# Kernel optimization log

Hardware: AMD Instinct MI355X
Metric: run time of the kernel (lower is better)

The kernel has to match this reference:

```python
import jax, jax.numpy as jnp
import numpy as np

B, T, D = 4, 2048, 1024
H = 4                      # fla GatedLinearAttention default num_heads
K = D; V = D               # expand_k = expand_v = 1
DK = K // H; DV = V // H   # 256 each
LOW = 16                   # gate_low_rank_dim default
GLN = 16.0                 # gate_logit_normalizer default


def _layernorm(x, w, b, eps=1e-5):
    mu = x.mean(-1, keepdims=True)
    xc = x - mu
    var = (xc * xc).mean(-1, keepdims=True)
    return xc * jax.lax.rsqrt(var + eps) * w + b


def _rmsnorm(x, w, eps=1e-5):
    ms = (x * x).mean(-1, keepdims=True)
    return x * jax.lax.rsqrt(ms + eps) * w


def _gla_scan(q, k, v, gk):
    # q,k,gk: [B,T,H,DK]; v: [B,T,H,DV]
    scale = DK ** -0.5
    qT = jnp.moveaxis(q * scale, 1, 0)  # [T,B,H,DK]
    kT = jnp.moveaxis(k, 1, 0)
    vT = jnp.moveaxis(v, 1, 0)
    gT = jnp.moveaxis(gk, 1, 0)

    def step(h, inp):
        qt, kt, vt, gt = inp  # [B,H,DK]/[B,H,DV]
        h = h * jnp.exp(gt)[..., None] + kt[..., :, None] * vt[..., None, :]
        o = jnp.einsum('bhk,bhkv->bhv', qt, h)
        return h, o

    h0 = jnp.zeros((q.shape[0], H, DK, DV), q.dtype)
    _, oT = jax.lax.scan(step, h0, (qT, kT, vT, gT))
    return jnp.moveaxis(oT, 0, 1)  # [B,T,H,DV]


def setup_inputs() -> dict:
    key = jax.random.key(0)
    ks = jax.random.split(key, 12)
    rn = lambda k, s: jax.random.normal(k, s, jnp.float32) * 0.02
    return {
        'x': jax.random.normal(ks[0], (B, T, D), jnp.float32),
        'ln1_w': jnp.ones((D,), jnp.float32), 'ln1_b': jnp.zeros((D,), jnp.float32),
        'Wq': rn(ks[1], (D, K)), 'Wk': rn(ks[2], (D, K)), 'Wv': rn(ks[3], (D, V)),
        'Wg': rn(ks[4], (D, V)),
        'Wgk1': rn(ks[5], (D, LOW)), 'Wgk2': rn(ks[6], (LOW, K)), 'bgk2': jnp.zeros((K,), jnp.float32),
        'rms_w': jnp.ones((DV,), jnp.float32),
        'Wo': rn(ks[7], (V, D)),
        'ln2_w': jnp.ones((D,), jnp.float32), 'ln2_b': jnp.zeros((D,), jnp.float32),
        'W1': rn(ks[8], (D, 3 * D)), 'b1': jnp.zeros((3 * D,), jnp.float32),
        'W2': rn(ks[9], (3 * D, D)), 'b2': jnp.zeros((D,), jnp.float32),
    }


def reference(x, ln1_w, ln1_b, Wq, Wk, Wv, Wg, Wgk1, Wgk2, bgk2, rms_w, Wo,
              ln2_w, ln2_b, W1, b1, W2, b2):
    b, t = x.shape[0], x.shape[1]
    xn = _layernorm(x, ln1_w, ln1_b)
    q = (xn @ Wq).reshape(b, t, H, DK)
    k = (xn @ Wk).reshape(b, t, H, DK)
    v = (xn @ Wv).reshape(b, t, H, DV)
    # low-rank forget gate: logsigmoid / gate_logit_normalizer
    gk = (jax.nn.log_sigmoid((xn @ Wgk1) @ Wgk2 + bgk2) / GLN).reshape(b, t, H, DK)
    o = _gla_scan(q, k, v, gk)                      # [B,T,H,DV]
    g = (xn @ Wg).reshape(b, t, H, DV)              # output gate
    o = _rmsnorm(o, rms_w) * (g * jax.nn.sigmoid(g))  # gated RMSNorm (swish gate)
    o = o.reshape(b, t, V) @ Wo
    x = x + o
    xn2 = _layernorm(x, ln2_w, ln2_b)
    h = jax.nn.leaky_relu(xn2 @ W1 + b1, 0.01)
    h = h * h                                        # LeakyReLU^2
    x = x + (h @ W2 + b2)
    return x
```

## Files before the change

kernel.cpp:

```cpp
#include <hip/hip_runtime.h>
#include <math.h>

#define BB 4
#define TT 2048
#define DD 1024
#define HH 4
#define DK 256
#define DV 256
#define RR 8192
#define CHK 64
#define NCHK 32
#define SS ((size_t)RR * DD)

typedef __bf16 bf16x8 __attribute__((ext_vector_type(8)));
typedef float f32x4 __attribute__((ext_vector_type(4)));

static __device__ inline unsigned short f2bf(float f) {
  unsigned int u = __float_as_uint(f);
  unsigned int r = (u + 0x7fffu + ((u >> 16) & 1u)) >> 16;
  return (unsigned short)r;
}
static __device__ inline float bf2f(unsigned short h) {
  return __uint_as_float(((unsigned int)h) << 16);
}

static __device__ __forceinline__ void gload16(const unsigned short* g,
                                               unsigned short* l) {
  __builtin_amdgcn_global_load_lds(
      (const __attribute__((address_space(1))) void*)g,
      (__attribute__((address_space(3))) void*)l, 16, 0, 0);
}

__global__ __launch_bounds__(256) void ln_kernel(const float* __restrict__ x,
                                                 const float* __restrict__ w,
                                                 const float* __restrict__ b,
                                                 unsigned short* __restrict__ yb) {
  int row = blockIdx.x;
  const float* xr = x + (size_t)row * DD;
  unsigned short* ybr = yb + (size_t)row * DD;
  int tid = threadIdx.x;

  float4 v = ((const float4*)xr)[tid];
  float s = v.x + v.y + v.z + v.w;
  float ss = v.x * v.x + v.y * v.y + v.z * v.z + v.w * v.w;
#pragma unroll
  for (int o = 32; o > 0; o >>= 1) {
    s += __shfl_down(s, o);
    ss += __shfl_down(ss, o);
  }
  __shared__ float ls[4], lss[4];
  int wid = tid >> 6;
  if ((tid & 63) == 0) { ls[wid] = s; lss[wid] = ss; }
  __syncthreads();
  float sum = ls[0] + ls[1] + ls[2] + ls[3];
  float sumsq = lss[0] + lss[1] + lss[2] + lss[3];
  float mu = sum * (1.0f / DD);
  float var = sumsq * (1.0f / DD) - mu * mu;
  float rs = rsqrtf(var + 1e-5f);

  float4 wv = ((const float4*)w)[tid];
  float4 bv = ((const float4*)b)[tid];
  ushort4 ob;
  ob.x = f2bf((v.x - mu) * rs * wv.x + bv.x);
  ob.y = f2bf((v.y - mu) * rs * wv.y + bv.y);
  ob.z = f2bf((v.z - mu) * rs * wv.z + bv.z);
  ob.w = f2bf((v.w - mu) * rs * wv.w + bv.w);
  ((ushort4*)ybr)[tid] = ob;
}

__global__ __launch_bounds__(256) void transpose_cast(const float* __restrict__ W,
                                                      unsigned short* __restrict__ Wt,
                                                      int K, int N) {
  __shared__ float t[32][33];
  int k0 = blockIdx.y * 32, n0 = blockIdx.x * 32;
  int tid = threadIdx.x;
  int tx = tid & 31, ty = tid >> 5;
#pragma unroll
  for (int i = 0; i < 4; ++i)
    t[ty + i * 8][tx] = W[(size_t)(k0 + ty + i * 8) * N + n0 + tx];
  __syncthreads();
#pragma unroll
  for (int i = 0; i < 4; ++i)
    Wt[(size_t)(n0 + ty + i * 8) * K + k0 + tx] = f2bf(t[tx][ty + i * 8]);
}

struct P5 {
  const float* w[5];
  unsigned short* o[5];
};
__global__ __launch_bounds__(256) void transpose5(P5 p) {
  __shared__ float t[32][33];
  int z = blockIdx.z;
  const float* W = p.w[z];
  unsigned short* Wt = p.o[z];
  int k0 = blockIdx.y * 32, n0 = blockIdx.x * 32;
  int tid = threadIdx.x;
  int tx = tid & 31, ty = tid >> 5;
#pragma unroll
  for (int i = 0; i < 4; ++i)
    t[ty + i * 8][tx] = W[(size_t)(k0 + ty + i * 8) * 1024 + n0 + tx];
  __syncthreads();
#pragma unroll
  for (int i = 0; i < 4; ++i)
    Wt[(size_t)(n0 + ty + i * 8) * 1024 + k0 + tx] = f2bf(t[tx][ty + i * 8]);
}

template <int EPI, int OUTBF>
__global__ __launch_bounds__(256) void gemm_bf16(
    const unsigned short* __restrict__ A,
    const unsigned short* __restrict__ Bt,
    const float* __restrict__ bias, const float* __restrict__ Res,
    void* __restrict__ Cv, int M, int N, int K) {
  __shared__ unsigned short As[2][128 * 64];
  __shared__ unsigned short Bs[2][128 * 64];
  int tid = threadIdx.x;
  int nwg = gridDim.x * gridDim.y;
  int wg = blockIdx.y * gridDim.x + blockIdx.x;
  int cpx = nwg >> 3;
  wg = (wg & 7) * cpx + (wg >> 3);
  int m0 = (wg / gridDim.x) * 128, n0 = (wg % gridDim.x) * 128;
  int lane = tid & 63;
  int w64 = tid & 192;
  int wid = tid >> 6;
  int wm = (wid >> 1) * 64, wn = (wid & 1) * 64;
  int fr = lane & 15, fq = lane >> 4;

  f32x4 acc[4][4] = {};

  auto STAGE = [&](int buf, int k0) {
#pragma unroll
    for (int j = 0; j < 4; ++j) {
      int gl = j * 256 + tid;
      int row = gl >> 3;
      int gs = (gl & 7) ^ (row & 7);
      gload16(&A[(size_t)(m0 + row) * K + k0 + gs * 8],
              &As[buf][(size_t)(j * 256 + w64) * 8]);
      gload16(&Bt[(size_t)(n0 + row) * K + k0 + gs * 8],
              &Bs[buf][(size_t)(j * 256 + w64) * 8]);
    }
  };

  STAGE(0, 0);
  asm volatile("s_waitcnt vmcnt(0)");
  __syncthreads();

  int cur = 0;
  for (int k0 = 0; k0 < K; k0 += 64) {
    if (k0 + 64 < K) STAGE(cur ^ 1, k0 + 64);

#pragma unroll
    for (int ph = 0; ph < 2; ++ph) {
      bf16x8 af[4], bv[4];
#pragma unroll
      for (int i = 0; i < 4; ++i) {
        int ra = wm + i * 16 + fr;
        af[i] = *(const bf16x8*)&As[cur][ra * 64 + (((ph * 4 + fq) ^ (ra & 7)) * 8)];
        int rb = wn + i * 16 + fr;
        bv[i] = *(const bf16x8*)&Bs[cur][rb * 64 + (((ph * 4 + fq) ^ (rb & 7)) * 8)];
      }
#pragma unroll
      for (int i = 0; i < 4; ++i)
#pragma unroll
        for (int jj = 0; jj < 4; ++jj)
          acc[i][jj] = __builtin_amdgcn_mfma_f32_16x16x32_bf16(af[i], bv[jj],
                                                               acc[i][jj], 0, 0, 0);
    }
    __syncthreads();
    cur ^= 1;
  }

  int col = lane & 15;
  int rbase = (lane >> 4) * 4;
#pragma unroll
  for (int i = 0; i < 4; ++i) {
#pragma unroll
    for (int j = 0; j < 4; ++j) {
      int n = n0 + wn + j * 16 + col;
      float bvv = (EPI == 2 || EPI == 4) ? bias[n] : 0.0f;
#pragma unroll
      for (int r = 0; r < 4; ++r) {
        int m = m0 + wm + i * 16 + rbase + r;
        float vv = acc[i][j][r] + bvv;
        if (EPI == 2) {
          float t = vv > 0.0f ? vv : 0.01f * vv;
          vv = t * t;
        }
        if (EPI == 3 || EPI == 4) vv += Res[(size_t)m * N + n];
        if (EPI == 5) {
          ((unsigned short*)Cv)[(size_t)(n >> 10) * SS + (size_t)m * 1024 +
                                (n & 1023)] = f2bf(vv);
        } else if (OUTBF) {
          ((unsigned short*)Cv)[(size_t)m * N + n] = f2bf(vv);
        } else {
          ((float*)Cv)[(size_t)m * N + n] = vv;
        }
      }
    }
  }
}

__global__ __launch_bounds__(256) void gk_kernel(const unsigned short* __restrict__ xn,
                                                 const float* __restrict__ Wgk1,
                                                 const float* __restrict__ Wgk2,
                                                 const float* __restrict__ bgk2,
                                                 unsigned short* __restrict__ gk) {
  __shared__ unsigned short Xs[16 * 1024];
  __shared__ unsigned short W1s[1024 * 16];
  __shared__ float Ts[16][16];
  int r0 = blockIdx.x * 16;
  int tid = threadIdx.x;

#pragma unroll
  for (int i = 0; i < 16; ++i) {
    int idx = tid + i * 256;
    ((ushort4*)Xs)[idx] = ((const ushort4*)(xn + (size_t)r0 * 1024))[idx];
  }
#pragma unroll
  for (int i = 0; i < 16; ++i) {
    int idx = tid + i * 256;
    float4 w = ((const float4*)Wgk1)[idx];
    ushort4 hh;
    hh.x = f2bf(w.x); hh.y = f2bf(w.y); hh.z = f2bf(w.z); hh.w = f2bf(w.w);
    ((ushort4*)W1s)[idx] = hh;
  }
  __syncthreads();

  {
    int r = tid >> 4, part = tid & 15;
    float t16[16];
#pragma unroll
    for (int j = 0; j < 16; ++j) t16[j] = 0.0f;
    for (int dd = 0; dd < 64; ++dd) {
      int d = dd * 16 + part;
      float xv = bf2f(Xs[r * 1024 + d]);
      const ushort4* wr = (const ushort4*)&W1s[d * 16];
#pragma unroll
      for (int q4 = 0; q4 < 4; ++q4) {
        ushort4 w = wr[q4];
        t16[q4 * 4 + 0] += xv * bf2f(w.x);
        t16[q4 * 4 + 1] += xv * bf2f(w.y);
        t16[q4 * 4 + 2] += xv * bf2f(w.z);
        t16[q4 * 4 + 3] += xv * bf2f(w.w);
      }
    }
#pragma unroll
    for (int j = 0; j < 16; ++j) {
      float s = t16[j];
      s += __shfl_xor(s, 1);
      s += __shfl_xor(s, 2);
      s += __shfl_xor(s, 4);
      s += __shfl_xor(s, 8);
      t16[j] = s;
    }
    if (part == 0) {
#pragma unroll
      for (int j = 0; j < 16; ++j) Ts[r][j] = t16[j];
    }
  }
  __syncthreads();

  {
    float w2[16][4];
#pragma unroll
    for (int j = 0; j < 16; ++j) {
      float4 wv = *(const float4*)&Wgk2[(size_t)j * 1024 + tid * 4];
      w2[j][0] = wv.x; w2[j][1] = wv.y; w2[j][2] = wv.z; w2[j][3] = wv.w;
    }
    float4 bv = *(const float4*)&bgk2[tid * 4];
    float bb[4] = {bv.x, bv.y, bv.z, bv.w};
#pragma unroll
    for (int r = 0; r < 16; ++r) {
      ushort4 outv;
      unsigned short* op = (unsigned short*)&outv;
#pragma unroll
      for (int jj = 0; jj < 4; ++jj) {
        float z = bb[jj];
#pragma unroll
        for (int j = 0; j < 16; ++j) z += Ts[r][j] * w2[j][jj];
        float lsg = fminf(z, 0.0f) - log1pf(expf(-fabsf(z)));
        op[jj] = f2bf(lsg * (1.0f / 16.0f));
      }
      *(ushort4*)&Xs[r * 1024 + tid * 4] = outv;
    }
  }
  __syncthreads();
#pragma unroll
  for (int i = 0; i < 16; ++i) {
    int idx = tid + i * 256;
    ((ushort4*)(gk + (size_t)r0 * 1024))[idx] = ((const ushort4*)Xs)[idx];
  }
}

__global__ __launch_bounds__(256) void gate_chunk(const unsigned short* __restrict__ gk,
                                                  unsigned short* __restrict__ q,
                                                  unsigned short* __restrict__ k,
                                                  float* __restrict__ ebC) {
  int bid = blockIdx.x;
  int c = bid & 31;
  int h = (bid >> 5) & 3;
  int b = bid >> 7;
  int tid = threadIdx.x;
  size_t base = ((size_t)b * TT + c * CHK) * 1024 + h * 256 + tid;

  float cums[64];
#pragma unroll
  for (int t = 0; t < 64; ++t) cums[t] = bf2f(gk[base + (size_t)t * 1024]);
  float cum = 0.0f;
#pragma unroll
  for (int t = 0; t < 64; ++t) {
    cum += cums[t];
    cums[t] = cum;
  }
  ebC[((b * 4 + h) * NCHK + c) * 256 + tid] = expf(cum);

  const float scale = 0.0625f;
#pragma unroll
  for (int t = 0; t < 64; ++t) {
    size_t a = base + (size_t)t * 1024;
    q[a] = f2bf(bf2f(q[a]) * expf(cums[t]) * scale);
    k[a] = f2bf(bf2f(k[a]) * expf(-cums[t]));
  }
}

template <int WITHE>
__global__ __launch_bounds__(256) void trans_kernel(const unsigned short* __restrict__ in,
                                                    const float* __restrict__ ebC,
                                                    unsigned short* __restrict__ outT) {
  __shared__ unsigned short T[64][68];
  int bid = blockIdx.x;
  int dkt = bid & 3;
  int ct = (bid >> 2) & 31;
  int bh = bid >> 7;
  int b = bh >> 2, h = bh & 3;
  int tid = threadIdx.x;
  int r = tid >> 4;
  int c4 = (tid & 15) * 4;
  size_t srcbase = ((size_t)b * TT + ct * 64) * 1024 + h * 256 + dkt * 64;
#pragma unroll
  for (int i = 0; i < 4; ++i)
    *(ushort4*)&T[r + i * 16][c4] =
        *(const ushort4*)&in[srcbase + (size_t)(r + i * 16) * 1024 + c4];
  __syncthreads();
  size_t outbase = (size_t)bh * 524288 + (size_t)(dkt * 64) * 2048 + ct * 64;
  const float* ep = ebC + ((size_t)bh * 32 + ct) * 256 + dkt * 64;
#pragma unroll
  for (int i = 0; i < 4; ++i) {
    int dkl = r + i * 16;
    float e = WITHE ? ep[dkl] : 1.0f;
    ushort4 o;
    o.x = f2bf(bf2f(T[c4 + 0][dkl]) * e);
    o.y = f2bf(bf2f(T[c4 + 1][dkl]) * e);
    o.z = f2bf(bf2f(T[c4 + 2][dkl]) * e);
    o.w = f2bf(bf2f(T[c4 + 3][dkl]) * e);
    *(ushort4*)&outT[outbase + (size_t)dkl * 2048 + c4] = o;
  }
}

__global__ __launch_bounds__(256) void u_gemm(const unsigned short* __restrict__ khatT,
                                              const unsigned short* __restrict__ vT,
                                              unsigned short* __restrict__ UT) {
  __shared__ unsigned short As[128 * 64];
  __shared__ unsigned short Bs[128 * 64];
  int tid = threadIdx.x;
  int bid = blockIdx.x;
  int tile = bid & 3;
  int bhc = bid >> 2;
  int bh = bhc >> 5, c = bhc & 31;
  int m0 = (tile >> 1) * 128, n0 = (tile & 1) * 128;
  const unsigned short* Ab = vT + (size_t)bh * 524288 + c * 64;
  const unsigned short* Bb = khatT + (size_t)bh * 524288 + c * 64;
  unsigned short* Cb = UT + (size_t)bhc * 65536;

  int lane = tid & 63;
  int w64 = tid & 192;
  int wid = tid >> 6;
  int wm = (wid >> 1) * 64, wn = (wid & 1) * 64;
  int fr = lane & 15, fq = lane >> 4;

  f32x4 acc[4][4] = {};

#pragma unroll
  for (int j = 0; j < 4; ++j) {
    int gl = j * 256 + tid;
    int row = gl >> 3;
    int gs = (gl & 7) ^ (row & 7);
    gload16(&Ab[(size_t)(m0 + row) * 2048 + gs * 8],
            &As[(size_t)(j * 256 + w64) * 8]);
    gload16(&Bb[(size_t)(n0 + row) * 2048 + gs * 8],
            &Bs[(size_t)(j * 256 + w64) * 8]);
  }
  __syncthreads();

#pragma unroll
  for (int ph = 0; ph < 2; ++ph) {
    bf16x8 af[4], bv[4];
#pragma unroll
    for (int i = 0; i < 4; ++i) {
      int ra = wm + i * 16 + fr;
      af[i] = *(const bf16x8*)&As[ra * 64 + (((ph * 4 + fq) ^ (ra & 7)) * 8)];
      int rb = wn + i * 16 + fr;
      bv[i] = *(const bf16x8*)&Bs[rb * 64 + (((ph * 4 + fq) ^ (rb & 7)) * 8)];
    }
#pragma unroll
    for (int i = 0; i < 4; ++i)
#pragma unroll
      for (int jj = 0; jj < 4; ++jj)
        acc[i][jj] = __builtin_amdgcn_mfma_f32_16x16x32_bf16(af[i], bv[jj],
                                                             acc[i][jj], 0, 0, 0);
  }

  int col = lane & 15;
  int rbase = (lane >> 4) * 4;
#pragma unroll
  for (int i = 0; i < 4; ++i)
#pragma unroll
    for (int j = 0; j < 4; ++j) {
      int n = n0 + wn + j * 16 + col;
#pragma unroll
      for (int r = 0; r < 4; ++r) {
        int m = m0 + wm + i * 16 + rbase + r;
        Cb[(size_t)m * 256 + n] = f2bf(acc[i][j][r]);
      }
    }
}

__global__ __launch_bounds__(256) void hscan(unsigned short* __restrict__ UH,
                                             const float* __restrict__ ebC) {
  int bid = blockIdx.x;
  int bh = bid >> 8, dv = bid & 255;
  int tid = threadIdx.x;
  size_t base = ((size_t)bh * NCHK) * 65536 + (size_t)dv * 256 + tid;
  const float* ebb = ebC + (size_t)bh * NCHK * 256 + tid;

  float u[32], e[32];
#pragma unroll
  for (int c = 0; c < 32; ++c) u[c] = bf2f(UH[base + (size_t)c * 65536]);
#pragma unroll
  for (int c = 0; c < 32; ++c) e[c] = ebb[c * 256];
  float h = 0.0f;
#pragma unroll
  for (int c = 0; c < 32; ++c) {
    UH[base + (size_t)c * 65536] = f2bf(h);
    h = e[c] * h + u[c];
  }
}

__global__ __launch_bounds__(256) void attn_fused(
    const unsigned short* __restrict__ qt, const unsigned short* __restrict__ kt,
    const unsigned short* __restrict__ vT, const unsigned short* __restrict__ HT,
    const unsigned short* __restrict__ gp, const float* __restrict__ rw,
    unsigned short* __restrict__ og) {
  __shared__ unsigned short Qs[64 * 264];
  __shared__ unsigned short KVH[256 * 72];
  __shared__ unsigned short Sb[64 * 64];
  __shared__ float red[64][4];

  int bid = blockIdx.x;
  int c = bid & 31;
  int bh = bid >> 5;
  int b = bh >> 2, h = bh & 3;
  size_t rowbase = ((size_t)b * TT + c * 64) * 1024 + h * 256;
  size_t vtbase = (size_t)bh * 524288 + c * 64;
  size_t htbase = ((size_t)(bh * 32 + c)) * 65536;
  int tid = threadIdx.x;
  int lane = tid & 63;
  int w = tid >> 6;
  int fr = lane & 15, fq = lane >> 4;

#pragma unroll
  for (int i = 0; i < 8; ++i) {
    int gg = tid + i * 256;
    int row = gg >> 5, gc = gg & 31;
    *(bf16x8*)&Qs[row * 264 + gc * 8] =
        *(const bf16x8*)&qt[rowbase + (size_t)row * 1024 + gc * 8];
    *(bf16x8*)&KVH[row * 264 + gc * 8] =
        *(const bf16x8*)&kt[rowbase + (size_t)row * 1024 + gc * 8];
  }
  __syncthreads();

  {
    f32x4 accs[4] = {};
#pragma unroll
    for (int ks = 0; ks < 8; ++ks) {
      bf16x8 af = *(const bf16x8*)&Qs[(w * 16 + fr) * 264 + ks * 32 + fq * 8];
#pragma unroll
      for (int si = 0; si < 4; ++si) {
        bf16x8 bf_ = *(const bf16x8*)&KVH[(si * 16 + fr) * 264 + ks * 32 + fq * 8];
        accs[si] = __builtin_amdgcn_mfma_f32_16x16x32_bf16(af, bf_, accs[si], 0, 0, 0);
      }
    }
#pragma unroll
    for (int si = 0; si < 4; ++si) {
#pragma unroll
      for (int r = 0; r < 4; ++r) {
        int t = w * 16 + fq * 4 + r;
        int s = si * 16 + fr;
        float val = (s <= t) ? accs[si][r] : 0.0f;
        Sb[t * 64 + (((s >> 3) ^ (t & 7)) * 8) + (s & 7)] = f2bf(val);
      }
    }
  }
  __syncthreads();

#pragma unroll
  for (int i = 0; i < 8; ++i) {
    int gg = tid + i * 256;
    int dv = gg >> 3, gc = gg & 7;
    *(bf16x8*)&KVH[dv * 72 + gc * 8] =
        *(const bf16x8*)&vT[vtbase + (size_t)dv * 2048 + gc * 8];
  }
  __syncthreads();

  int dv0 = w * 64;
  f32x4 acc[4][4] = {};

#pragma unroll
  for (int ks = 0; ks < 2; ++ks) {
    bf16x8 af[4], bv[4];
#pragma unroll
    for (int ti = 0; ti < 4; ++ti) {
      int t = ti * 16 + fr;
      af[ti] = *(const bf16x8*)&Sb[t * 64 + (((ks * 4 + fq) ^ (t & 7)) * 8)];
    }
#pragma unroll
    for (int nj = 0; nj < 4; ++nj)
      bv[nj] = *(const bf16x8*)&KVH[(dv0 + nj * 16 + fr) * 72 + ks * 32 + fq * 8];
#pragma unroll
    for (int ti = 0; ti < 4; ++ti)
#pragma unroll
      for (int nj = 0; nj < 4; ++nj)
        acc[ti][nj] = __builtin_amdgcn_mfma_f32_16x16x32_bf16(af[ti], bv[nj],
                                                              acc[ti][nj], 0, 0, 0);
  }

  for (int k4 = 0; k4 < 4; ++k4) {
    __syncthreads();
#pragma unroll
    for (int i = 0; i < 8; ++i) {
      int gg = tid + i * 256;
      int dv = gg >> 3, gc = gg & 7;
      *(bf16x8*)&KVH[dv * 72 + gc * 8] =
          *(const bf16x8*)&HT[htbase + (size_t)dv * 256 + k4 * 64 + gc * 8];
    }
    __syncthreads();
#pragma unroll
    for (int ks = 0; ks < 2; ++ks) {
      bf16x8 af[4], bv[4];
#pragma unroll
      for (int ti = 0; ti < 4; ++ti)
        af[ti] = *(const bf16x8*)&Qs[(ti * 16 + fr) * 264 + k4 * 64 + ks * 32 + fq * 8];
#pragma unroll
      for (int nj = 0; nj < 4; ++nj)
        bv[nj] = *(const bf16x8*)&KVH[(dv0 + nj * 16 + fr) * 72 + ks * 32 + fq * 8];
#pragma unroll
      for (int ti = 0; ti < 4; ++ti)
#pragma unroll
        for (int nj = 0; nj < 4; ++nj)
          acc[ti][nj] = __builtin_amdgcn_mfma_f32_16x16x32_bf16(af[ti], bv[nj],
                                                                acc[ti][nj], 0, 0, 0);
    }
  }

  float rstd[4][4];
#pragma unroll
  for (int ti = 0; ti < 4; ++ti) {
#pragma unroll
    for (int r = 0; r < 4; ++r) {
      float s = 0.0f;
#pragma unroll
      for (int nj = 0; nj < 4; ++nj) {
        float v = acc[ti][nj][r];
        s += v * v;
      }
      s += __shfl_xor(s, 1);
      s += __shfl_xor(s, 2);
      s += __shfl_xor(s, 4);
      s += __shfl_xor(s, 8);
      rstd[ti][r] = s;
    }
  }
  if (fr == 0) {
#pragma unroll
    for (int ti = 0; ti < 4; ++ti)
#pragma unroll
      for (int r = 0; r < 4; ++r)
        red[ti * 16 + fq * 4 + r][w] = rstd[ti][r];
  }
  __syncthreads();
#pragma unroll
  for (int ti = 0; ti < 4; ++ti) {
#pragma unroll
    for (int r = 0; r < 4; ++r) {
      int t = ti * 16 + fq * 4 + r;
      float tot = red[t][0] + red[t][1] + red[t][2] + red[t][3];
      rstd[ti][r] = rsqrtf(tot * (1.0f / 256.0f) + 1e-5f);
    }
  }
#pragma unroll
  for (int ti = 0; ti < 4; ++ti) {
#pragma unroll
    for (int nj = 0; nj < 4; ++nj) {
      int dv = dv0 + nj * 16 + fr;
      float rwv = rw[dv];
#pragma unroll
      for (int r = 0; r < 4; ++r) {
        int t = ti * 16 + fq * 4 + r;
        float gv = bf2f(gp[rowbase + (size_t)t * 1024 + dv]);
        float sw = gv / (1.0f + expf(-gv));
        og[rowbase + (size_t)t * 1024 + dv] =
            f2bf(acc[ti][nj][r] * rstd[ti][r] * rwv * sw);
      }
    }
  }
}

extern "C" void kernel_launch(void* const* d_in, const int* in_sizes, int n_in,
                              void* d_out, int out_size, void* d_ws,
                              size_t ws_size, hipStream_t stream) {
  const float* x = (const float*)d_in[0];
  const float* ln1_w = (const float*)d_in[1];
  const float* ln1_b = (const float*)d_in[2];
  const float* Wq = (const float*)d_in[3];
  const float* Wk = (const float*)d_in[4];
  const float* Wv = (const float*)d_in[5];
  const float* Wg = (const float*)d_in[6];
  const float* Wgk1 = (const float*)d_in[7];
  const float* Wgk2 = (const float*)d_in[8];
  const float* bgk2 = (const float*)d_in[9];
  const float* rms_w = (const float*)d_in[10];
  const float* Wo = (const float*)d_in[11];
  const float* ln2_w = (const float*)d_in[12];
  const float* ln2_b = (const float*)d_in[13];
  const float* W1 = (const float*)d_in[14];
  const float* b1 = (const float*)d_in[15];
  const float* W2 = (const float*)d_in[16];
  const float* b2 = (const float*)d_in[17];
  float* out = (float*)d_out;

  const size_t S = SS;
  unsigned short* actb = (unsigned short*)d_ws;
  unsigned short* qb = actb + S;
  unsigned short* kb = qb + S;
  unsigned short* vb = kb + S;
  unsigned short* gb = vb + S;
  unsigned short* gkb = gb + S;
  unsigned short* ogb = gkb + S;
  unsigned short* UH = ogb + 2 * S;
  float* ebC = (float*)(UH + 4 * S);
  unsigned short* Wqkvgt = (unsigned short*)(ebC + 131072);
  unsigned short* Wot = Wqkvgt + 4194304;
  unsigned short* W1t = Wot + 1048576;
  unsigned short* W2t = W1t + 3145728;
  unsigned short* khatT = gkb;
  unsigned short* vT = actb;
  float* x1 = (float*)kb;
  unsigned short* hb = UH;

  dim3 blk(256);

  P5 p5;
  p5.w[0] = Wq;  p5.o[0] = Wqkvgt;
  p5.w[1] = Wk;  p5.o[1] = Wqkvgt + 1048576;
  p5.w[2] = Wv;  p5.o[2] = Wqkvgt + 2097152;
  p5.w[3] = Wg;  p5.o[3] = Wqkvgt + 3145728;
  p5.w[4] = Wo;  p5.o[4] = Wot;
  transpose5<<<dim3(32, 32, 5), blk, 0, stream>>>(p5);
  transpose_cast<<<dim3(96, 32), blk, 0, stream>>>(W1, W1t, 1024, 3072);
  transpose_cast<<<dim3(32, 96), blk, 0, stream>>>(W2, W2t, 3072, 1024);

  ln_kernel<<<RR, blk, 0, stream>>>(x, ln1_w, ln1_b, actb);

  dim3 g4096(4096 / 128, RR / 128);
  gemm_bf16<5, 1><<<g4096, blk, 0, stream>>>(actb, Wqkvgt, nullptr, nullptr, qb,
                                             RR, 4096, 1024);

  gk_kernel<<<RR / 16, blk, 0, stream>>>(actb, Wgk1, Wgk2, bgk2, gkb);

  gate_chunk<<<BB * HH * NCHK, blk, 0, stream>>>(gkb, qb, kb, ebC);

  trans_kernel<1><<<16 * 32 * 4, blk, 0, stream>>>(kb, ebC, khatT);
  trans_kernel<0><<<16 * 32 * 4, blk, 0, stream>>>(vb, ebC, vT);

  u_gemm<<<16 * NCHK * 4, blk, 0, stream>>>(khatT, vT, UH);
  hscan<<<16 * 256, blk, 0, stream>>>(UH, ebC);

  attn_fused<<<16 * NCHK, blk, 0, stream>>>(qb, kb, vT, UH, gb, rms_w, ogb);

  dim3 g1024(1024 / 128, RR / 128);
  gemm_bf16<3, 0><<<g1024, blk, 0, stream>>>(ogb, Wot, nullptr, x, x1, RR, 1024, 1024);

  ln_kernel<<<RR, blk, 0, stream>>>(x1, ln2_w, ln2_b, actb);

  dim3 g3072(3072 / 128, RR / 128);
  gemm_bf16<2, 1><<<g3072, blk, 0, stream>>>(actb, W1t, b1, nullptr, hb, RR, 3072, 1024);

  gemm_bf16<4, 0><<<g1024, blk, 0, stream>>>(hb, W2t, b2, x1, out, RR, 1024, 3072);
}
```

Measured before the change: 426.1 us.

## Replace 128x128 GEMM with 256x256-tile, 512-thread software-pipelined MFMA kernel

Replaces the bf16 GEMM used for the QKVG, output, and both MLP projections with a 256x256 output tile computed by 8 waves. Loads are split into half-tile stages interleaved with the MFMA phases, with explicit barriers, waitcnt, sched_barrier and setprio to overlap global-to-LDS copies with compute. The aim is more data reuse per loaded tile and better latency hiding. In exchange it uses 128KB of LDS, holds 128 accumulator registers per lane, launches fewer workgroups (only 128 for the N=1024 GEMMs), and depends on fragile hand-written synchronisation.

```diff
diff --git a/kernel.cpp b/kernel.cpp
--- a/kernel.cpp
+++ b/kernel.cpp
@@ -106,73 +106,118 @@
 }
 
 template <int EPI, int OUTBF>
-__global__ __launch_bounds__(256) void gemm_bf16(
+__global__ __launch_bounds__(512, 2) void gemm256(
     const unsigned short* __restrict__ A,
     const unsigned short* __restrict__ Bt,
     const float* __restrict__ bias, const float* __restrict__ Res,
     void* __restrict__ Cv, int M, int N, int K) {
-  __shared__ unsigned short As[2][128 * 64];
-  __shared__ unsigned short Bs[2][128 * 64];
+  __shared__ unsigned short As[2][2][128 * 64];
+  __shared__ unsigned short Bs[2][2][128 * 64];
   int tid = threadIdx.x;
   int nwg = gridDim.x * gridDim.y;
   int wg = blockIdx.y * gridDim.x + blockIdx.x;
   int cpx = nwg >> 3;
   wg = (wg & 7) * cpx + (wg >> 3);
-  int m0 = (wg / gridDim.x) * 128, n0 = (wg % gridDim.x) * 128;
+  int m0 = (wg / gridDim.x) * 256, n0 = (wg % gridDim.x) * 256;
   int lane = tid & 63;
-  int w64 = tid & 192;
+  int w64 = tid & 448;
   int wid = tid >> 6;
-  int wm = (wid >> 1) * 64, wn = (wid & 1) * 64;
+  int wm = (wid >> 2) * 128;
+  int wn = (wid & 3) * 64;
   int fr = lane & 15, fq = lane >> 4;
 
-  f32x4 acc[4][4] = {};
-
-  auto STAGE = [&](int buf, int k0) {
-#pragma unroll
-    for (int j = 0; j < 4; ++j) {
-      int gl = j * 256 + tid;
+  f32x4 acc[8][4] = {};
+  int nt = K >> 6;
+
+  auto STAGEH = [&](int mat, int h, int t) {
+    if (t >= nt) return;
+    int d = t & 1;
+    const unsigned short* G = mat ? Bt : A;
+    int base0 = (mat ? n0 : m0) + h * 128;
+    unsigned short* L = mat ? &Bs[d][h][0] : &As[d][h][0];
+    int k0 = t * 64;
+#pragma unroll
+    for (int j = 0; j < 2; ++j) {
+      int gl = j * 512 + tid;
       int row = gl >> 3;
       int gs = (gl & 7) ^ (row & 7);
-      gload16(&A[(size_t)(m0 + row) * K + k0 + gs * 8],
-              &As[buf][(size_t)(j * 256 + w64) * 8]);
-      gload16(&Bt[(size_t)(n0 + row) * K + k0 + gs * 8],
-              &Bs[buf][(size_t)(j * 256 + w64) * 8]);
+      gload16(&G[(size_t)(base0 + row) * K + k0 + gs * 8],
+              &L[(size_t)(j * 512 + w64) * 8]);
     }
   };
 
-  STAGE(0, 0);
-  asm volatile("s_waitcnt vmcnt(0)");
-  __syncthreads();
-
-  int cur = 0;
-  for (int k0 = 0; k0 < K; k0 += 64) {
-    if (k0 + 64 < K) STAGE(cur ^ 1, k0 + 64);
-
-#pragma unroll
-    for (int ph = 0; ph < 2; ++ph) {
-      bf16x8 af[4], bv[4];
-#pragma unroll
-      for (int i = 0; i < 4; ++i) {
-        int ra = wm + i * 16 + fr;
-        af[i] = *(const bf16x8*)&As[cur][ra * 64 + (((ph * 4 + fq) ^ (ra & 7)) * 8)];
-        int rb = wn + i * 16 + fr;
-        bv[i] = *(const bf16x8*)&Bs[cur][rb * 64 + (((ph * 4 + fq) ^ (rb & 7)) * 8)];
-      }
-#pragma unroll
-      for (int i = 0; i < 4; ++i)
-#pragma unroll
-        for (int jj = 0; jj < 4; ++jj)
-          acc[i][jj] = __builtin_amdgcn_mfma_f32_16x16x32_bf16(af[i], bv[jj],
-                                                               acc[i][jj], 0, 0, 0);
-    }
-    __syncthreads();
-    cur ^= 1;
+  STAGEH(0, 0, 0); STAGEH(0, 1, 0);
+  STAGEH(1, 0, 0); STAGEH(1, 1, 0);
+  STAGEH(1, 0, 1); STAGEH(1, 1, 1);
+  asm volatile("s_waitcnt vmcnt(0)" ::: "memory");
+  __builtin_amdgcn_sched_barrier(0);
+  __builtin_amdgcn_s_barrier();
+  __builtin_amdgcn_sched_barrier(0);
+
+  for (int u = 0; u < nt; u += 2) {
+#pragma unroll
+    for (int hh = 0; hh < 2; ++hh) {
+      int d = hh;
+      bf16x8 breg[4][2];
+#pragma unroll
+      for (int p = 0; p < 4; ++p) {
+        bf16x8 af[2][2];
+        if (p == 0) {
+#pragma unroll
+          for (int j = 0; j < 4; ++j) {
+            int rb = wn + j * 16 + fr;
+            int hB = rb >> 7, rr = rb & 127;
+#pragma unroll
+            for (int ks = 0; ks < 2; ++ks)
+              breg[j][ks] = *(const bf16x8*)&Bs[d][hB][rr * 64 +
+                                (((ks * 4 + fq) ^ (rr & 7)) * 8)];
+          }
+        }
+#pragma unroll
+        for (int i = 0; i < 2; ++i) {
+          int ra = wm + (2 * p + i) * 16 + fr;
+          int hA = ra >> 7, rr = ra & 127;
+#pragma unroll
+          for (int ks = 0; ks < 2; ++ks)
+            af[i][ks] = *(const bf16x8*)&As[d][hA][rr * 64 +
+                              (((ks * 4 + fq) ^ (rr & 7)) * 8)];
+        }
+        if (hh == 0) {
+          if (p == 0) STAGEH(0, 0, u + 1);
+          if (p == 1) { STAGEH(0, 1, u + 1); STAGEH(1, 0, u + 2); }
+          if (p == 2) STAGEH(1, 1, u + 2);
+        } else {
+          if (p == 0) STAGEH(0, 0, u + 2);
+          if (p == 1) STAGEH(0, 1, u + 2);
+          if (p == 2) STAGEH(1, 0, u + 3);
+          if (p == 3) STAGEH(1, 1, u + 3);
+        }
+        __builtin_amdgcn_sched_barrier(0);
+        __builtin_amdgcn_s_barrier();
+        asm volatile("s_waitcnt lgkmcnt(0)" ::: "memory");
+        __builtin_amdgcn_sched_barrier(0);
+        __builtin_amdgcn_s_setprio(1);
+#pragma unroll
+        for (int i = 0; i < 2; ++i)
+#pragma unroll
+          for (int j = 0; j < 4; ++j)
+#pragma unroll
+            for (int ks = 0; ks < 2; ++ks)
+              acc[2 * p + i][j] = __builtin_amdgcn_mfma_f32_16x16x32_bf16(
+                  af[i][ks], breg[j][ks], acc[2 * p + i][j], 0, 0, 0);
+        __builtin_amdgcn_s_setprio(0);
+        if (p == 3) asm volatile("s_waitcnt vmcnt(4)" ::: "memory");
+        __builtin_amdgcn_sched_barrier(0);
+        __builtin_amdgcn_s_barrier();
+        __builtin_amdgcn_sched_barrier(0);
+      }
+    }
   }
 
   int col = lane & 15;
   int rbase = (lane >> 4) * 4;
 #pragma unroll
-  for (int i = 0; i < 4; ++i) {
+  for (int i = 0; i < 8; ++i) {
 #pragma unroll
     for (int j = 0; j < 4; ++j) {
       int n = n0 + wn + j * 16 + col;
@@ -182,8 +227,8 @@
         int m = m0 + wm + i * 16 + rbase + r;
         float vv = acc[i][j][r] + bvv;
         if (EPI == 2) {
-          float t = vv > 0.0f ? vv : 0.01f * vv;
-          vv = t * t;
+          float t2 = vv > 0.0f ? vv : 0.01f * vv;
+          vv = t2 * t2;
         }
         if (EPI == 3 || EPI == 4) vv += Res[(size_t)m * N + n];
         if (EPI == 5) {
@@ -657,6 +702,7 @@
   unsigned short* hb = UH;
 
   dim3 blk(256);
+  dim3 blk512(512);
 
   P5 p5;
   p5.w[0] = Wq;  p5.o[0] = Wqkvgt;
@@ -670,9 +716,9 @@
 
   ln_kernel<<<RR, blk, 0, stream>>>(x, ln1_w, ln1_b, actb);
 
-  dim3 g4096(4096 / 128, RR / 128);
-  gemm_bf16<5, 1><<<g4096, blk, 0, stream>>>(actb, Wqkvgt, nullptr, nullptr, qb,
-                                             RR, 4096, 1024);
+  dim3 g4096(4096 / 256, RR / 256);
+  gemm256<5, 1><<<g4096, blk512, 0, stream>>>(actb, Wqkvgt, nullptr, nullptr, qb,
+                                              RR, 4096, 1024);
 
   gk_kernel<<<RR / 16, blk, 0, stream>>>(actb, Wgk1, Wgk2, bgk2, gkb);
 
@@ -686,13 +732,13 @@
 
   attn_fused<<<16 * NCHK, blk, 0, stream>>>(qb, kb, vT, UH, gb, rms_w, ogb);
 
-  dim3 g1024(1024 / 128, RR / 128);
-  gemm_bf16<3, 0><<<g1024, blk, 0, stream>>>(ogb, Wot, nullptr, x, x1, RR, 1024, 1024);
+  dim3 g1024(1024 / 256, RR / 256);
+  gemm256<3, 0><<<g1024, blk512, 0, stream>>>(ogb, Wot, nullptr, x, x1, RR, 1024, 1024);
 
   ln_kernel<<<RR, blk, 0, stream>>>(x1, ln2_w, ln2_b, actb);
 
-  dim3 g3072(3072 / 128, RR / 128);
-  gemm_bf16<2, 1><<<g3072, blk, 0, stream>>>(actb, W1t, b1, nullptr, hb, RR, 3072, 1024);
-
-  gemm_bf16<4, 0><<<g1024, blk, 0, stream>>>(hb, W2t, b2, x1, out, RR, 1024, 3072);
-}
+  dim3 g3072(3072 / 256, RR / 256);
+  gemm256<2, 1><<<g3072, blk512, 0, stream>>>(actb, W1t, b1, nullptr, hb, RR, 3072, 1024);
+
+  gemm256<4, 0><<<g1024, blk512, 0, stream>>>(hb, W2t, b2, x1, out, RR, 1024, 3072);
+}
```

New measurement: 453.8 us. +6.5%, slower.

## Fuse chunk state GEMM and scan into one kernel; shrink GEMM K-tile

Applied to the files above, without the earlier changes.

The separate per-chunk U GEMM and the hidden-state scan are replaced by one kernel. Each block owns a 64x64 (dv, dk) tile of the state and walks the 32 chunks in order. It computes the chunk update with MFMA, keeps the running state in fp32 registers and writes each chunk's prefix state. This removes the round trip of writing the U buffer to global memory and reading it back, and drops a launch. The cost is only 256 blocks with a serial chunk loop, which exposes per-chunk latency. Separately, the main bf16 GEMM K-step drops from 64 to 32, halving shared memory per block to allow more resident blocks, at the cost of twice as many barriers and loop iterations.

```diff
diff --git a/kernel.cpp b/kernel.cpp
--- a/kernel.cpp
+++ b/kernel.cpp
@@ -111,8 +111,8 @@
     const unsigned short* __restrict__ Bt,
     const float* __restrict__ bias, const float* __restrict__ Res,
     void* __restrict__ Cv, int M, int N, int K) {
-  __shared__ unsigned short As[2][128 * 64];
-  __shared__ unsigned short Bs[2][128 * 64];
+  __shared__ unsigned short As[2][128 * 32];
+  __shared__ unsigned short Bs[2][128 * 32];
   int tid = threadIdx.x;
   int nwg = gridDim.x * gridDim.y;
   int wg = blockIdx.y * gridDim.x + blockIdx.x;
@@ -129,10 +129,10 @@
 
   auto STAGE = [&](int buf, int k0) {
 #pragma unroll
-    for (int j = 0; j < 4; ++j) {
+    for (int j = 0; j < 2; ++j) {
       int gl = j * 256 + tid;
-      int row = gl >> 3;
-      int gs = (gl & 7) ^ (row & 7);
+      int row = gl >> 2;
+      int gs = (gl & 3) ^ (row & 3);
       gload16(&A[(size_t)(m0 + row) * K + k0 + gs * 8],
               &As[buf][(size_t)(j * 256 + w64) * 8]);
       gload16(&Bt[(size_t)(n0 + row) * K + k0 + gs * 8],
@@ -145,26 +145,23 @@
   __syncthreads();
 
   int cur = 0;
-  for (int k0 = 0; k0 < K; k0 += 64) {
-    if (k0 + 64 < K) STAGE(cur ^ 1, k0 + 64);
-
-#pragma unroll
-    for (int ph = 0; ph < 2; ++ph) {
-      bf16x8 af[4], bv[4];
-#pragma unroll
-      for (int i = 0; i < 4; ++i) {
-        int ra = wm + i * 16 + fr;
-        af[i] = *(const bf16x8*)&As[cur][ra * 64 + (((ph * 4 + fq) ^ (ra & 7)) * 8)];
-        int rb = wn + i * 16 + fr;
-        bv[i] = *(const bf16x8*)&Bs[cur][rb * 64 + (((ph * 4 + fq) ^ (rb & 7)) * 8)];
-      }
-#pragma unroll
-      for (int i = 0; i < 4; ++i)
-#pragma unroll
-        for (int jj = 0; jj < 4; ++jj)
-          acc[i][jj] = __builtin_amdgcn_mfma_f32_16x16x32_bf16(af[i], bv[jj],
-                                                               acc[i][jj], 0, 0, 0);
-    }
+  for (int k0 = 0; k0 < K; k0 += 32) {
+    if (k0 + 32 < K) STAGE(cur ^ 1, k0 + 32);
+
+    bf16x8 af[4], bv[4];
+#pragma unroll
+    for (int i = 0; i < 4; ++i) {
+      int ra = wm + i * 16 + fr;
+      af[i] = *(const bf16x8*)&As[cur][ra * 32 + ((fq ^ (ra & 3)) * 8)];
+      int rb = wn + i * 16 + fr;
+      bv[i] = *(const bf16x8*)&Bs[cur][rb * 32 + ((fq ^ (rb & 3)) * 8)];
+    }
+#pragma unroll
+    for (int i = 0; i < 4; ++i)
+#pragma unroll
+      for (int jj = 0; jj < 4; ++jj)
+        acc[i][jj] = __builtin_amdgcn_mfma_f32_16x16x32_bf16(af[i], bv[jj],
+                                                             acc[i][jj], 0, 0, 0);
     __syncthreads();
     cur ^= 1;
   }
@@ -356,92 +353,86 @@
   }
 }
 
-__global__ __launch_bounds__(256) void u_gemm(const unsigned short* __restrict__ khatT,
-                                              const unsigned short* __restrict__ vT,
-                                              unsigned short* __restrict__ UT) {
-  __shared__ unsigned short As[128 * 64];
-  __shared__ unsigned short Bs[128 * 64];
-  int tid = threadIdx.x;
+__global__ __launch_bounds__(256) void ustate_kernel(
+    const unsigned short* __restrict__ khatT, const unsigned short* __restrict__ vT,
+    const float* __restrict__ ebC, unsigned short* __restrict__ HT) {
+  __shared__ unsigned short Vs[2][64 * 72];
+  __shared__ unsigned short Ks[2][64 * 72];
   int bid = blockIdx.x;
-  int tile = bid & 3;
-  int bhc = bid >> 2;
-  int bh = bhc >> 5, c = bhc & 31;
-  int m0 = (tile >> 1) * 128, n0 = (tile & 1) * 128;
-  const unsigned short* Ab = vT + (size_t)bh * 524288 + c * 64;
-  const unsigned short* Bb = khatT + (size_t)bh * 524288 + c * 64;
-  unsigned short* Cb = UT + (size_t)bhc * 65536;
-
+  int tile = bid & 15;
+  int bh = bid >> 4;
+  int dv0 = (tile >> 2) * 64, dk0 = (tile & 3) * 64;
+  const unsigned short* Vb = vT + (size_t)bh * 524288 + (size_t)dv0 * 2048;
+  const unsigned short* Kb = khatT + (size_t)bh * 524288 + (size_t)dk0 * 2048;
+  int tid = threadIdx.x;
   int lane = tid & 63;
-  int w64 = tid & 192;
-  int wid = tid >> 6;
-  int wm = (wid >> 1) * 64, wn = (wid & 1) * 64;
+  int w = tid >> 6;
   int fr = lane & 15, fq = lane >> 4;
 
-  f32x4 acc[4][4] = {};
-
-#pragma unroll
-  for (int j = 0; j < 4; ++j) {
-    int gl = j * 256 + tid;
-    int row = gl >> 3;
-    int gs = (gl & 7) ^ (row & 7);
-    gload16(&Ab[(size_t)(m0 + row) * 2048 + gs * 8],
-            &As[(size_t)(j * 256 + w64) * 8]);
-    gload16(&Bb[(size_t)(n0 + row) * 2048 + gs * 8],
-            &Bs[(size_t)(j * 256 + w64) * 8]);
-  }
-  __syncthreads();
-
-#pragma unroll
-  for (int ph = 0; ph < 2; ++ph) {
-    bf16x8 af[4], bv[4];
-#pragma unroll
-    for (int i = 0; i < 4; ++i) {
-      int ra = wm + i * 16 + fr;
-      af[i] = *(const bf16x8*)&As[ra * 64 + (((ph * 4 + fq) ^ (ra & 7)) * 8)];
-      int rb = wn + i * 16 + fr;
-      bv[i] = *(const bf16x8*)&Bs[rb * 64 + (((ph * 4 + fq) ^ (rb & 7)) * 8)];
-    }
-#pragma unroll
-    for (int i = 0; i < 4; ++i)
-#pragma unroll
-      for (int jj = 0; jj < 4; ++jj)
-        acc[i][jj] = __builtin_amdgcn_mfma_f32_16x16x32_bf16(af[i], bv[jj],
-                                                             acc[i][jj], 0, 0, 0);
-  }
-
-  int col = lane & 15;
-  int rbase = (lane >> 4) * 4;
-#pragma unroll
-  for (int i = 0; i < 4; ++i)
-#pragma unroll
-    for (int j = 0; j < 4; ++j) {
-      int n = n0 + wn + j * 16 + col;
+  bf16x8 vr[2], kr[2], nvr[2], nkr[2];
+  auto LOADR = [&](int c, bf16x8 vv[2], bf16x8 kk[2]) {
+#pragma unroll
+    for (int j = 0; j < 2; ++j) {
+      int g = j * 256 + tid;
+      int row = g >> 3, gc = g & 7;
+      vv[j] = *(const bf16x8*)&Vb[(size_t)row * 2048 + c * 64 + gc * 8];
+      kk[j] = *(const bf16x8*)&Kb[(size_t)row * 2048 + c * 64 + gc * 8];
+    }
+  };
+  auto WLDS = [&](int buf, bf16x8 vv[2], bf16x8 kk[2]) {
+#pragma unroll
+    for (int j = 0; j < 2; ++j) {
+      int g = j * 256 + tid;
+      int row = g >> 3, gc = g & 7;
+      *(bf16x8*)&Vs[buf][row * 72 + gc * 8] = vv[j];
+      *(bf16x8*)&Ks[buf][row * 72 + gc * 8] = kk[j];
+    }
+  };
+
+  f32x4 st[4] = {};
+
+  LOADR(0, vr, kr);
+  WLDS(0, vr, kr);
+  __syncthreads();
+
+  for (int c = 0; c < NCHK; ++c) {
+    int cur = c & 1;
+    if (c + 1 < NCHK) LOADR(c + 1, nvr, nkr);
+
+    size_t hb = ((size_t)(bh * NCHK + c)) * 65536;
+#pragma unroll
+    for (int nj = 0; nj < 4; ++nj) {
 #pragma unroll
       for (int r = 0; r < 4; ++r) {
-        int m = m0 + wm + i * 16 + rbase + r;
-        Cb[(size_t)m * 256 + n] = f2bf(acc[i][j][r]);
-      }
-    }
-}
-
-__global__ __launch_bounds__(256) void hscan(unsigned short* __restrict__ UH,
-                                             const float* __restrict__ ebC) {
-  int bid = blockIdx.x;
-  int bh = bid >> 8, dv = bid & 255;
-  int tid = threadIdx.x;
-  size_t base = ((size_t)bh * NCHK) * 65536 + (size_t)dv * 256 + tid;
-  const float* ebb = ebC + (size_t)bh * NCHK * 256 + tid;
-
-  float u[32], e[32];
-#pragma unroll
-  for (int c = 0; c < 32; ++c) u[c] = bf2f(UH[base + (size_t)c * 65536]);
-#pragma unroll
-  for (int c = 0; c < 32; ++c) e[c] = ebb[c * 256];
-  float h = 0.0f;
-#pragma unroll
-  for (int c = 0; c < 32; ++c) {
-    UH[base + (size_t)c * 65536] = f2bf(h);
-    h = e[c] * h + u[c];
+        int dv = dv0 + w * 16 + fq * 4 + r;
+        int dk = dk0 + nj * 16 + fr;
+        HT[hb + (size_t)dv * 256 + dk] = f2bf(st[nj][r]);
+      }
+    }
+
+    f32x4 uacc[4] = {};
+#pragma unroll
+    for (int ks = 0; ks < 2; ++ks) {
+      bf16x8 av = *(const bf16x8*)&Vs[cur][(w * 16 + fr) * 72 + ks * 32 + fq * 8];
+#pragma unroll
+      for (int nj = 0; nj < 4; ++nj) {
+        bf16x8 bk = *(const bf16x8*)&Ks[cur][(nj * 16 + fr) * 72 + ks * 32 + fq * 8];
+        uacc[nj] = __builtin_amdgcn_mfma_f32_16x16x32_bf16(av, bk, uacc[nj], 0, 0, 0);
+      }
+    }
+
+    const float* ec = ebC + ((size_t)bh * NCHK + c) * 256 + dk0;
+#pragma unroll
+    for (int nj = 0; nj < 4; ++nj) {
+      float e = ec[nj * 16 + fr];
+      st[nj] = e * st[nj] + uacc[nj];
+    }
+
+    __syncthreads();
+    if (c + 1 < NCHK) {
+      WLDS(cur ^ 1, nvr, nkr);
+      __syncthreads();
+    }
   }
 }
 
@@ -681,8 +672,7 @@
   trans_kernel<1><<<16 * 32 * 4, blk, 0, stream>>>(kb, ebC, khatT);
   trans_kernel<0><<<16 * 32 * 4, blk, 0, stream>>>(vb, ebC, vT);
 
-  u_gemm<<<16 * NCHK * 4, blk, 0, stream>>>(khatT, vT, UH);
-  hscan<<<16 * 256, blk, 0, stream>>>(UH, ebC);
+  ustate_kernel<<<16 * 16, blk, 0, stream>>>(khatT, vT, ebC, UH);
 
   attn_fused<<<16 * NCHK, blk, 0, stream>>>(qb, kb, vT, UH, gb, rms_w, ogb);
 
```

After: 439.2 us. 1.03x slower.
